# Kernel tuning notes

Hardware: AMD Instinct MI355X
Metric: run time of the kernel (lower is better)

## Reference

```python
import jax, jax.numpy as jnp
import numpy as np

N, C, E, B, NPG, MAX_LEN, H, EF = 16384, 512, 524288, 64, 256, 512, 8, 16
EPS = 1e-5

def layernorm(x, g, b):
    m = jnp.mean(x, axis=-1, keepdims=True)
    v = jnp.mean(jnp.square(x - m), axis=-1, keepdims=True)
    return (x - m) / jnp.sqrt(v + EPS) * g + b

def setup_inputs() -> dict:
    key = jax.random.key(0)
    ks = list(jax.random.split(key, 32))
    x = jax.random.normal(ks[0], (N, C), dtype=jnp.float32)
    edge_attr = jax.random.normal(ks[1], (E, EF), dtype=jnp.float32)
    # edges within each graph of NPG nodes
    src = jax.random.randint(ks[2], (E,), 0, N)
    dst = (src // NPG) * NPG + jax.random.randint(ks[3], (E,), 0, NPG)
    edge_index = jnp.stack([src, dst]).astype(jnp.int64)
    batch = jnp.repeat(jnp.arange(B), NPG).astype(jnp.int64)  # sorted graph ids
    s = 0.03
    p = lambda k, shp: jax.random.normal(k, shp, dtype=jnp.float32) * s
    return dict(
        x=x, edge_attr=edge_attr,
        gcn_w=p(ks[4], (C, C)), gcn_b=jnp.zeros((C,)),
        ep_w=p(ks[5], (EF, C)), ep_b=jnp.zeros((C,)),
        gate_w=p(ks[6], (2 * C, C)), gate_b=jnp.zeros((C,)),
        n1_g=jnp.ones((C,)), n1_b=jnp.zeros((C,)),
        in_w=p(ks[7], (C, 3 * C)), in_b=jnp.zeros((3 * C,)),
        out_w=p(ks[8], (C, C)), out_b=jnp.zeros((C,)),
        tn_g=jnp.ones((C,)), tn_b=jnp.zeros((C,)),
        m_w1=p(ks[9], (C, 2 * C)), m_b1=jnp.zeros((2 * C,)),
        m_w2=p(ks[10], (2 * C, C)), m_b2=jnp.zeros((C,)),
        fn_g=jnp.ones((C,)), fn_b=jnp.zeros((C,)),
        edge_index=edge_index, batch=batch,
    )

def reference(x, edge_attr, gcn_w, gcn_b, ep_w, ep_b, gate_w, gate_b,
              n1_g, n1_b, in_w, in_b, out_w, out_b, tn_g, tn_b,
              m_w1, m_b1, m_w2, m_b2, fn_g, fn_b, edge_index, batch):
    src, dst = edge_index[0], edge_index[1]
    # --- CoGNN: weighted GCN conv (self-loops, sym norm) ---
    ew = jax.lax.stop_gradient(jnp.sqrt(jnp.sum(edge_attr * edge_attr, axis=-1)))
    loop = jnp.arange(N)
    src2 = jnp.concatenate([src, loop]); dst2 = jnp.concatenate([dst, loop])
    ew2 = jnp.concatenate([ew, jnp.ones((N,), ew.dtype)])
    deg = jax.ops.segment_sum(ew2, dst2, num_segments=N)
    dinv = jnp.where(deg > 0, jax.lax.rsqrt(jnp.maximum(deg, 1e-12)), 0.0)
    norm = dinv[src2] * ew2 * dinv[dst2]
    xw = x @ gcn_w
    x_conv = jax.ops.segment_sum(norm[:, None] * xw[src2], dst2, num_segments=N) + gcn_b
    # edge_proj -> scatter_add at source nodes (dropout = identity in eval)
    ef = jax.nn.relu(edge_attr @ ep_w + ep_b)
    ef = jax.ops.segment_sum(ef, src, num_segments=N)
    gate = jax.nn.sigmoid(jnp.concatenate([x_conv, ef], axis=-1) @ gate_w + gate_b)
    x1 = gate * x_conv + (1.0 - gate) * ef
    x1 = jax.nn.relu(layernorm(x1, n1_g, n1_b))
    x = x1 + x  # identity residual (in_channels == hidden_channels)
    # --- to_dense_batch ---
    counts = jax.ops.segment_sum(jnp.ones((N,), jnp.int32), batch, num_segments=B)
    starts = jnp.cumsum(counts) - counts
    pos = jnp.arange(N) - starts[batch]
    xd = jnp.zeros((B, MAX_LEN, C), x.dtype).at[batch, pos].set(x)
    maskd = jnp.zeros((B, MAX_LEN), bool).at[batch, pos].set(True)
    # --- MHA (batch_first, key_padding_mask = ~mask) ---
    Dh = C // H
    qkv = xd @ in_w + in_b
    q, k, v = jnp.split(qkv, 3, axis=-1)
    q = q.reshape(B, MAX_LEN, H, Dh); k = k.reshape(B, MAX_LEN, H, Dh); v = v.reshape(B, MAX_LEN, H, Dh)
    scores = jnp.einsum('blhd,bmhd->bhlm', q, k) / jnp.sqrt(jnp.asarray(Dh, x.dtype))
    scores = jnp.where(maskd[:, None, None, :], scores, -1e9)
    attn = jax.nn.softmax(scores, axis=-1)
    o = jnp.einsum('bhlm,bmhd->blhd', attn, v).reshape(B, MAX_LEN, C)
    o = o @ out_w + out_b
    x_global = o[batch, pos]  # undo dense batching: x_global[mask]
    x = layernorm(x + x_global, tn_g, tn_b)
    # --- MLP ---
    x = x + (jax.nn.silu(x @ m_w1 + m_b1) @ m_w2 + m_b2)
    return layernorm(x, fn_g, fn_b)
```

## Files before the change

kernel.cpp:

```cpp
#include <hip/hip_runtime.h>

#define NN 16384
#define CC 512
#define EE 524288
#define BB 64
#define HH 8
#define EFD 16
#define GEMAXE 10240

typedef __bf16 bf16_t;
typedef __bf16 bf16x4 __attribute__((ext_vector_type(4)));
typedef __bf16 bf16x8 __attribute__((ext_vector_type(8)));
typedef float f32x4v __attribute__((ext_vector_type(4)));

__device__ __forceinline__ float2 ldb2(const bf16_t* p) {
  unsigned w = *(const unsigned*)p;
  return make_float2(__uint_as_float(w << 16), __uint_as_float(w & 0xFFFF0000u));
}


__global__ void init_kernel(int* ghist, int* nid_src, bf16_t* eacsr) {
  int i = threadIdx.x;
  if (i < 64) ghist[i] = 0;
  if (i < 32) nid_src[EE + i] = -1;
  ((int*)(eacsr + (size_t)EE * 16))[i] = 0;
}

__global__ __launch_bounds__(256) void edge_pass1(const float* __restrict__ ea,
                                                  const int* __restrict__ dst,
                                                  float* __restrict__ ew, int* ghist) {
  __shared__ int h[64];
  int tid = threadIdx.x;
  if (tid < 64) h[tid] = 0;
  __syncthreads();
  int e = blockIdx.x * 256 + tid;
  const float4* p = (const float4*)(ea + (size_t)e * EFD);
  float s = 0.f;
#pragma unroll
  for (int i = 0; i < 4; ++i) {
    float4 v = p[i];
    s += v.x * v.x + v.y * v.y + v.z * v.z + v.w * v.w;
  }
  ew[e] = sqrtf(s);
  atomicAdd(&h[dst[e] >> 8], 1);
  __syncthreads();
  if (tid < 64 && h[tid]) atomicAdd(&ghist[tid], h[tid]);
}

__global__ void gexscan_kernel(const int* __restrict__ ghist, int* __restrict__ gstart,
                               int* __restrict__ gcur) {
  if (threadIdx.x == 0) {
    int s = 0;
    for (int g = 0; g < 64; ++g) { gstart[g] = s; gcur[g] = s; s += ghist[g]; }
    gstart[64] = s;
  }
}

__global__ __launch_bounds__(256) void graph_scatter_kernel(
    const int* __restrict__ src, const int* __restrict__ dst,
    const float* __restrict__ ew, int* gcur, int2* __restrict__ grec,
    float* __restrict__ ewg) {
  __shared__ int h[64], base[64], h2[64];
  int tid = threadIdx.x;
  if (tid < 64) { h[tid] = 0; h2[tid] = 0; }
  __syncthreads();
  int e0 = blockIdx.x * 2048;
  int gloc[8];
#pragma unroll
  for (int k = 0; k < 8; ++k) {
    gloc[k] = dst[e0 + k * 256 + tid] >> 8;
    atomicAdd(&h[gloc[k]], 1);
  }
  __syncthreads();
  if (tid < 64) base[tid] = h[tid] ? atomicAdd(&gcur[tid], h[tid]) : 0;
  __syncthreads();
#pragma unroll
  for (int k = 0; k < 8; ++k) {
    int e = e0 + k * 256 + tid;
    int g = gloc[k];
    int p = atomicAdd(&h2[g], 1);
    int pos = base[g] + p;
    int ls = src[e] & 255;
    int ld = dst[e] & 255;
    grec[pos] = make_int2(e | (ls << 19), ld);
    ewg[pos] = ew[e];
  }
}

__global__ __launch_bounds__(1024) void graph_sort2_kernel(
    const int2* __restrict__ grec, const float* __restrict__ ewg,
    const int* __restrict__ gstart, int* __restrict__ elist_src,
    int* __restrict__ nid_src, int* __restrict__ start_src,
    float2* __restrict__ dstrec, int* __restrict__ start_dst,
    float* __restrict__ dinv) {
  __shared__ int lbuf[GEMAXE];
  __shared__ unsigned short sl[GEMAXE];
  __shared__ float ewl[GEMAXE];
  __shared__ int h[256], hx[256], h2[256];
  __shared__ float fdinv[256];
  const int g = blockIdx.x & 63;
  const int tid = threadIdx.x;
  const int gs = gstart[g];
  const int cnt = gstart[g + 1] - gs;
  if (tid < 256) { h[tid] = 0; h2[tid] = 0; }
  __syncthreads();
  if (blockIdx.x < 64) {
    for (int i = tid; i < cnt; i += 1024) {
      int2 r = grec[gs + i];
      int ld = r.y;
      sl[i] = (unsigned short)(((r.x >> 19) & 255) | (ld << 8));
      ewl[i] = ewg[gs + i];
      atomicAdd(&h[ld], 1);
    }
    __syncthreads();
    int myc = (tid < 256) ? h[tid] : 0;
    for (int off = 1; off < 256; off <<= 1) {
      int v = (tid < 256 && tid >= off) ? h[tid - off] : 0;
      __syncthreads();
      if (tid < 256) h[tid] += v;
      __syncthreads();
    }
    if (tid < 256) {
      hx[tid] = h[tid] - myc;
      start_dst[g * 256 + tid] = gs + hx[tid];
    }
    if (g == 63 && tid == 0) start_dst[NN] = EE;
    __syncthreads();
    for (int i = tid; i < cnt; i += 1024) {
      int ld = sl[i] >> 8;
      int p = hx[ld] + atomicAdd(&h2[ld], 1);
      lbuf[p] = i;
    }
    __syncthreads();
    if (tid < 256) {
      float dg = 1.0f;
      int s0 = hx[tid], e0 = s0 + myc;
      for (int i = s0; i < e0; ++i) dg += ewl[lbuf[i]];
      float dv = rsqrtf(fmaxf(dg, 1e-12f));
      fdinv[tid] = dv;
      dinv[g * 256 + tid] = dv;
    }
    __syncthreads();
    for (int p = tid; p < cnt; p += 1024) {
      int i = lbuf[p];
      int ls = sl[i] & 255;
      dstrec[gs + p] = make_float2(fdinv[ls] * ewl[i], __int_as_float(g * 256 + ls));
    }
  } else {
    int* wb = (int*)ewl;
    for (int i = tid; i < cnt; i += 1024) {
      int w = grec[gs + i].x;
      wb[i] = w;
      atomicAdd(&h[w >> 19], 1);
    }
    __syncthreads();
    int myc = (tid < 256) ? h[tid] : 0;
    for (int off = 1; off < 256; off <<= 1) {
      int v = (tid < 256 && tid >= off) ? h[tid - off] : 0;
      __syncthreads();
      if (tid < 256) h[tid] += v;
      __syncthreads();
    }
    if (tid < 256) {
      hx[tid] = h[tid] - myc;
      start_src[g * 256 + tid] = gs + hx[tid];
    }
    if (g == 63 && tid == 0) start_src[NN] = EE;
    __syncthreads();
    for (int i = tid; i < cnt; i += 1024) {
      int w = wb[i];
      int ls = w >> 19;
      int p = hx[ls] + atomicAdd(&h2[ls], 1);
      lbuf[p] = w;
    }
    __syncthreads();
    for (int p = tid; p < cnt; p += 1024) {
      int w = lbuf[p];
      elist_src[gs + p] = w & 0x7FFFF;
      nid_src[gs + p] = g * 256 + (w >> 19);
    }
  }
}

__global__ void ea_gather_kernel(const float* __restrict__ ea,
                                 const int* __restrict__ elist,
                                 bf16_t* __restrict__ eacsr) {
  int idx = blockIdx.x * 256 + threadIdx.x;
  if (idx >= EE * 2) return;
  int pos = idx >> 1, half = idx & 1;
  int e = elist[pos];
  const f32x4v* p = (const f32x4v*)(ea + (size_t)e * EFD + half * 8);
  f32x4v u0 = p[0], u1 = p[1];
  bf16x8 f;
#pragma unroll
  for (int r = 0; r < 4; ++r) {
    f[r] = (bf16_t)u0[r];
    f[4 + r] = (bf16_t)u1[r];
  }
  *(bf16x8*)(eacsr + (size_t)pos * 16 + half * 8) = f;
}


__global__ void cvt_bf16_kernel(const float* __restrict__ in, bf16_t* __restrict__ out,
                                int n4) {
  int i = blockIdx.x * 256 + threadIdx.x;
  if (i >= n4) return;
  float4 v = ((const float4*)in)[i];
  bf16x4 o;
  o[0] = (bf16_t)v.x; o[1] = (bf16_t)v.y; o[2] = (bf16_t)v.z; o[3] = (bf16_t)v.w;
  ((bf16x4*)out)[i] = o;
}

__global__ __launch_bounds__(256) void wt_kernel(const float* __restrict__ W,
                                                 bf16_t* __restrict__ Wt, int K, int N) {
  __shared__ float tile[32][33];
  int bx = blockIdx.x * 32;
  int by = blockIdx.y * 32;
  int tx = threadIdx.x & 31, ty = threadIdx.x >> 5;
#pragma unroll
  for (int i = 0; i < 32; i += 8)
    tile[ty + i][tx] = W[(size_t)(by + ty + i) * N + bx + tx];
  __syncthreads();
#pragma unroll
  for (int i = 0; i < 32; i += 8)
    Wt[(size_t)(bx + ty + i) * K + by + tx] = (bf16_t)tile[tx][ty + i];
}

__global__ __launch_bounds__(256) void xconv_kernel(
    const bf16_t* __restrict__ xwb, const float* __restrict__ dinv,
    const float2* __restrict__ dstrec, const int* __restrict__ start,
    const float* __restrict__ gcn_b, bf16_t* __restrict__ xcb) {
  int i = blockIdx.x;
  int tid = threadIdx.x;
  int st = start[i], en = start[i + 1];
  float di = dinv[i];
  int c0 = tid * 2;
  __shared__ float2 scS[256];
  float2 xv = ldb2(xwb + (size_t)i * CC + c0);
  float sc = di * di;
  float a0 = sc * xv.x + gcn_b[c0];
  float a1 = sc * xv.y + gcn_b[c0 + 1];
  for (int p0 = st; p0 < en; p0 += 256) {
    int m = min(256, en - p0);
    __syncthreads();
    if (tid < m) {
      float2 r = dstrec[p0 + tid];
      scS[tid] = make_float2(r.x * di, r.y);
    }
    __syncthreads();
    for (int j = 0; j < m; ++j) {
      float2 scv = scS[j];
      int sn = __float_as_int(scv.y);
      float2 v = ldb2(xwb + (size_t)sn * CC + c0);
      a0 += scv.x * v.x;
      a1 += scv.x * v.y;
    }
  }
  xcb[(size_t)i * (2 * CC) + c0] = (bf16_t)a0;
  xcb[(size_t)i * (2 * CC) + c0 + 1] = (bf16_t)a1;
}

__global__ __launch_bounds__(256) void ef_mfma_kernel(
    const bf16_t* __restrict__ eacsr, const float* __restrict__ ep_w,
    const float* __restrict__ ep_b, const int* __restrict__ nid,
    const int* __restrict__ start, bf16_t* __restrict__ efb) {
  const int tid = threadIdx.x;
  const int lane = tid & 63;
  const int wv = tid >> 6;
  const int l15 = lane & 15;
  const int g = lane >> 4;
  const int n0 = blockIdx.x * 16;
  const int cbase = wv * 128;

  bf16x8 wfr[8];
#pragma unroll
  for (int t = 0; t < 8; ++t) {
    bf16x8 f = {};
    int c = cbase + t * 16 + l15;
    if (g < 2) {
#pragma unroll
      for (int j = 0; j < 8; ++j) f[j] = (bf16_t)ep_w[(g * 8 + j) * CC + c];
    } else if (g == 2) {
      f[0] = (bf16_t)ep_b[c];
    }
    wfr[t] = f;
  }

  const int st = start[n0];
  const int en = start[n0 + 16];
  const int tgt = n0 + l15;

  f32x4v eacc[8] = {};

  for (int cb = st; cb < en; cb += 32) {
    bf16x8 af[2];
#pragma unroll
    for (int mE = 0; mE < 2; ++mE) {
      bf16x8 f = {};
      if (g < 2) {
        f = *(const bf16x8*)(eacsr + (size_t)(cb + mE * 16 + l15) * 16 + g * 8);
      } else if (g == 2) {
        f[0] = (bf16_t)1.0f;
      }
      af[mE] = f;
    }
    int4 idlo = *(const int4*)(nid + cb + g * 4);
    int4 idhi = *(const int4*)(nid + cb + 16 + g * 4);
    bf16x8 sf;
    sf[0] = (idlo.x == tgt) ? (bf16_t)1.0f : (bf16_t)0.0f;
    sf[1] = (idlo.y == tgt) ? (bf16_t)1.0f : (bf16_t)0.0f;
    sf[2] = (idlo.z == tgt) ? (bf16_t)1.0f : (bf16_t)0.0f;
    sf[3] = (idlo.w == tgt) ? (bf16_t)1.0f : (bf16_t)0.0f;
    sf[4] = (idhi.x == tgt) ? (bf16_t)1.0f : (bf16_t)0.0f;
    sf[5] = (idhi.y == tgt) ? (bf16_t)1.0f : (bf16_t)0.0f;
    sf[6] = (idhi.z == tgt) ? (bf16_t)1.0f : (bf16_t)0.0f;
    sf[7] = (idhi.w == tgt) ? (bf16_t)1.0f : (bf16_t)0.0f;
#pragma unroll
    for (int t = 0; t < 8; ++t) {
      f32x4v s0 = {}, s1 = {};
      s0 = __builtin_amdgcn_mfma_f32_16x16x32_bf16(af[0], wfr[t], s0, 0, 0, 0);
      s1 = __builtin_amdgcn_mfma_f32_16x16x32_bf16(af[1], wfr[t], s1, 0, 0, 0);
      union { bf16x8 v; bf16x4 h[2]; } pf;
#pragma unroll
      for (int r = 0; r < 4; ++r) {
        pf.h[0][r] = (bf16_t)fmaxf(s0[r], 0.f);
        pf.h[1][r] = (bf16_t)fmaxf(s1[r], 0.f);
      }
      eacc[t] = __builtin_amdgcn_mfma_f32_16x16x32_bf16(sf, pf.v, eacc[t], 0, 0, 0);
    }
  }
#pragma unroll
  for (int t = 0; t < 8; ++t) {
    int c = cbase + t * 16 + l15;
#pragma unroll
    for (int r = 0; r < 4; ++r) {
      int node = n0 + g * 4 + r;
      efb[(size_t)node * (2 * CC) + CC + c] = (bf16_t)eacc[t][r];
    }
  }
}

__device__ __forceinline__ void gl_lds16(const bf16_t* g, bf16_t* l) {
  __builtin_amdgcn_global_load_lds(
      (const __attribute__((address_space(1))) void*)g,
      (__attribute__((address_space(3))) void*)l, 16, 0, 0);
}

template <int ACT, int OUT>
__global__ __launch_bounds__(256) void gemm_bf16_kernel(
    const bf16_t* __restrict__ A, const bf16_t* __restrict__ Bt,
    const float* __restrict__ bias, void* __restrict__ Cout, int M, int N, int K) {
  __shared__ __align__(16) bf16_t Al[128 * 32];
  __shared__ __align__(16) bf16_t Bl[128 * 32];
  const int tid = threadIdx.x;
  const int lane = tid & 63;
  const int wave = tid >> 6;
  const int row0 = blockIdx.y * 128;
  const int col0 = blockIdx.x * 128;
  const int wm = (wave >> 1) * 64;
  const int wn = (wave & 1) * 64;
  f32x4v acc[4][4] = {};
  const bf16_t* aBase = A + (size_t)(row0 + (tid >> 2)) * K + (tid & 3) * 8;
  const bf16_t* bBase = Bt + (size_t)(col0 + (tid >> 2)) * K + (tid & 3) * 8;
  bf16_t* al0 = Al + wave * 512;
  bf16_t* al1 = Al + 2048 + wave * 512;
  bf16_t* bl0 = Bl + wave * 512;
  bf16_t* bl1 = Bl + 2048 + wave * 512;
  const int fr = lane & 15;
  const int fk = (lane >> 4) * 8;
  for (int k0 = 0; k0 < K; k0 += 32) {
    gl_lds16(aBase + k0, al0);
    gl_lds16(aBase + (size_t)64 * K + k0, al1);
    gl_lds16(bBase + k0, bl0);
    gl_lds16(bBase + (size_t)64 * K + k0, bl1);
    __syncthreads();
    bf16x8 af[4], bfv[4];
#pragma unroll
    for (int m = 0; m < 4; ++m)
      af[m] = *(const bf16x8*)(Al + (wm + m * 16 + fr) * 32 + fk);
#pragma unroll
    for (int n = 0; n < 4; ++n)
      bfv[n] = *(const bf16x8*)(Bl + (wn + n * 16 + fr) * 32 + fk);
#pragma unroll
    for (int m = 0; m < 4; ++m)
#pragma unroll
      for (int n = 0; n < 4; ++n)
        acc[m][n] =
            __builtin_amdgcn_mfma_f32_16x16x32_bf16(af[m], bfv[n], acc[m][n], 0, 0, 0);
    __syncthreads();
  }
  const int fq = (lane >> 4) * 4;
#pragma unroll
  for (int m = 0; m < 4; ++m) {
    int grb = row0 + wm + m * 16 + fq;
#pragma unroll
    for (int n = 0; n < 4; ++n) {
      int gc = col0 + wn + n * 16 + fr;
      float bv = bias ? bias[gc] : 0.f;
#pragma unroll
      for (int r = 0; r < 4; ++r) {
        float v = acc[m][n][r] + bv;
        if (ACT == 1) v = v / (1.f + __expf(-v));
        if (OUT == 0)
          ((float*)Cout)[(size_t)(grb + r) * N + gc] = v;
        else
          ((bf16_t*)Cout)[(size_t)(grb + r) * N + gc] = (bf16_t)v;
      }
    }
  }
}


__device__ inline void block_reduce2(float& s, float& q, float* red) {
#pragma unroll
  for (int off = 32; off >= 1; off >>= 1) {
    s += __shfl_xor(s, off, 64);
    q += __shfl_xor(q, off, 64);
  }
  int wid = threadIdx.x >> 6;
  if ((threadIdx.x & 63) == 0) { red[wid * 2] = s; red[wid * 2 + 1] = q; }
  __syncthreads();
  s = red[0] + red[2] + red[4] + red[6];
  q = red[1] + red[3] + red[5] + red[7];
}

template <int IA, int IB, int WF>
__global__ __launch_bounds__(256) void ln_addT_kernel(
    const void* __restrict__ A, const void* __restrict__ Bv,
    const float* __restrict__ g, const float* __restrict__ be,
    float* __restrict__ outf, bf16_t* __restrict__ outb) {
  int row = blockIdx.x, tid = threadIdx.x, c0 = tid * 2;
  __shared__ float red[8];
  float2 a = IA ? ldb2((const bf16_t*)A + (size_t)row * CC + c0)
                : *(const float2*)((const float*)A + (size_t)row * CC + c0);
  float2 b = IB ? ldb2((const bf16_t*)Bv + (size_t)row * CC + c0)
                : *(const float2*)((const float*)Bv + (size_t)row * CC + c0);
  float x0 = a.x + b.x, x1 = a.y + b.y;
  float s = x0 + x1, q = x0 * x0 + x1 * x1;
  block_reduce2(s, q, red);
  float mean = s * (1.f / CC);
  float var = q * (1.f / CC) - mean * mean;
  float rs = rsqrtf(var + 1e-5f);
  float o0 = (x0 - mean) * rs * g[c0] + be[c0];
  float o1 = (x1 - mean) * rs * g[c0 + 1] + be[c0 + 1];
  if (WF) {
    *(float2*)(outf + (size_t)row * CC + c0) = make_float2(o0, o1);
  } else {
    outb[(size_t)row * CC + c0] = (bf16_t)o0;
    outb[(size_t)row * CC + c0 + 1] = (bf16_t)o1;
  }
}

__global__ __launch_bounds__(256) void ln_gate_kernel(
    const bf16_t* __restrict__ gpreb, const float* __restrict__ gate_b,
    const bf16_t* __restrict__ xcef, const float* __restrict__ n1g,
    const float* __restrict__ n1b, const float* __restrict__ xin,
    bf16_t* __restrict__ x2b) {
  int row = blockIdx.x, tid = threadIdx.x, c0 = tid * 2;
  __shared__ float red[8];
  float2 gp = ldb2(gpreb + (size_t)row * CC + c0);
  float2 xcv = ldb2(xcef + (size_t)row * (2 * CC) + c0);
  float2 efv = ldb2(xcef + (size_t)row * (2 * CC) + CC + c0);
  float g0 = 1.f / (1.f + __expf(-(gp.x + gate_b[c0])));
  float g1 = 1.f / (1.f + __expf(-(gp.y + gate_b[c0 + 1])));
  float x0 = g0 * xcv.x + (1.f - g0) * efv.x;
  float x1 = g1 * xcv.y + (1.f - g1) * efv.y;
  float s = x0 + x1, q = x0 * x0 + x1 * x1;
  block_reduce2(s, q, red);
  float mean = s * (1.f / CC);
  float var = q * (1.f / CC) - mean * mean;
  float rs = rsqrtf(var + 1e-5f);
  float2 xi = *(const float2*)(xin + (size_t)row * CC + c0);
  float o0 = fmaxf((x0 - mean) * rs * n1g[c0] + n1b[c0], 0.f) + xi.x;
  float o1 = fmaxf((x1 - mean) * rs * n1g[c0 + 1] + n1b[c0 + 1], 0.f) + xi.y;
  x2b[(size_t)row * CC + c0] = (bf16_t)o0;
  x2b[(size_t)row * CC + c0 + 1] = (bf16_t)o1;
}

__global__ __launch_bounds__(256) void vt_pack_kernel(const bf16_t* __restrict__ qkvb,
                                                      bf16_t* __restrict__ vt) {
  int b = blockIdx.x >> 3, h = blockIdx.x & 7;
  int nb = b * 256;
  size_t voff = 1024 + (size_t)h * 64;
  char* out = (char*)(vt + (size_t)blockIdx.x * (64 * 256));
  __shared__ bf16_t tile[64][80];
  int tid = threadIdx.x;
  for (int kb = 0; kb < 4; ++kb) {
    __syncthreads();
#pragma unroll
    for (int p = 0; p < 2; ++p) {
      int k = p * 32 + (tid >> 3);
      int d8 = tid & 7;
      bf16x8 v = *(const bf16x8*)(qkvb + (size_t)(nb + kb * 64 + k) * 1536 + voff + d8 * 8);
      *(bf16x8*)(&tile[k][d8 * 8]) = v;
    }
    __syncthreads();
#pragma unroll
    for (int p = 0; p < 2; ++p) {
      int d = p * 32 + (tid >> 3);
      int k8 = tid & 7;
      bf16x8 v;
#pragma unroll
      for (int j = 0; j < 8; ++j) {
        int pos = k8 * 8 + j;
        int sl = pos & 31;
        int srck = (pos & 32) + ((sl >> 3) << 2) + (sl & 3) + (((sl >> 2) & 1) << 4);
        v[j] = tile[srck][d];
      }
      int byteoff = d * 512 + ((kb * 128 + k8 * 16) ^ ((d & 7) << 4));
      *(bf16x8*)(out + byteoff) = v;
    }
  }
}

__global__ __launch_bounds__(256, 2) void attn_mfma_kernel(
    const bf16_t* __restrict__ qkvb, const bf16_t* __restrict__ vt,
    bf16_t* __restrict__ o) {
  const int b = blockIdx.x >> 3;
  const int h = blockIdx.x & 7;
  const int nb = b * 256;
  const int tid = threadIdx.x;
  const int lane = tid & 63;
  const int wv = tid >> 6;
  const int l15 = lane & 15;
  const int g = lane >> 4;
  const int swzk = (l15 & 7) << 4;
  __shared__ __align__(16) bf16_t Klds[256 * 64];
  __shared__ __align__(16) bf16_t Vtlds[64 * 256];
  const size_t qoff = (size_t)h * 64;
  const size_t koff = 512 + (size_t)h * 64;

  {
    const int dcol = 16 * ((tid & 7) ^ ((tid >> 3) & 7));
    const bf16_t* srcb = qkvb + koff + (dcol >> 1);
#pragma unroll
    for (int i = 0; i < 8; ++i) {
      int k = i * 32 + (tid >> 3);
      gl_lds16(srcb + (size_t)(nb + k) * 1536, Klds + ((i * 4096 + wv * 1024) >> 1));
    }
  }
  {
    const bf16_t* vsrc = vt + (size_t)blockIdx.x * (64 * 256);
#pragma unroll
    for (int i = 0; i < 8; ++i) {
      int base = i * 4096 + wv * 1024;
      gl_lds16(vsrc + ((base >> 1) + lane * 8), Vtlds + (base >> 1));
    }
  }

  bf16x8 qf[4][2];
#pragma unroll
  for (int n = 0; n < 4; ++n) {
    const bf16_t* qp = qkvb + (size_t)(nb + wv * 64 + 16 * n + l15) * 1536 + qoff + g * 8;
    qf[n][0] = *(const bf16x8*)(qp);
    qf[n][1] = *(const bf16x8*)(qp + 32);
  }

  __syncthreads();

  f32x4v oacc[4][4] = {};
  float mrun[4] = {-1e30f, -1e30f, -1e30f, -1e30f};
  float lrun[4] = {0.f, 0.f, 0.f, 0.f};

  for (int kc = 0; kc < 4; ++kc) {
    f32x4v sacc[4][4] = {};
    const int kb128 = (kc * 64 + l15) * 128;
#pragma unroll
    for (int m = 0; m < 4; ++m) {
      bf16x8 a0 = *(const bf16x8*)(Klds + ((kb128 + m * 2048 + ((g * 16) ^ swzk)) >> 1));
      bf16x8 a1 =
          *(const bf16x8*)(Klds + ((kb128 + m * 2048 + ((64 + g * 16) ^ swzk)) >> 1));
#pragma unroll
      for (int n = 0; n < 4; ++n) {
        sacc[m][n] = __builtin_amdgcn_mfma_f32_16x16x32_bf16(a0, qf[n][0], sacc[m][n], 0, 0, 0);
        sacc[m][n] = __builtin_amdgcn_mfma_f32_16x16x32_bf16(a1, qf[n][1], sacc[m][n], 0, 0, 0);
      }
    }
    uint2 pb[4][4];
#pragma unroll
    for (int n = 0; n < 4; ++n) {
      float mx = sacc[0][n][0];
#pragma unroll
      for (int m = 0; m < 4; ++m)
#pragma unroll
        for (int r = 0; r < 4; ++r) mx = fmaxf(mx, sacc[m][n][r]);
      mx = fmaxf(mx, __shfl_xor(mx, 16));
      mx = fmaxf(mx, __shfl_xor(mx, 32));
      float mnew = fmaxf(mrun[n], mx);
      float c = __expf((mrun[n] - mnew) * 0.125f);
      mrun[n] = mnew;
      float s = 0.f;
#pragma unroll
      for (int m = 0; m < 4; ++m) {
        float p0 = __expf((sacc[m][n][0] - mnew) * 0.125f);
        float p1 = __expf((sacc[m][n][1] - mnew) * 0.125f);
        float p2 = __expf((sacc[m][n][2] - mnew) * 0.125f);
        float p3 = __expf((sacc[m][n][3] - mnew) * 0.125f);
        s += (p0 + p1) + (p2 + p3);
        union { bf16x4 v; uint2 u; } cv;
        cv.v[0] = (bf16_t)p0; cv.v[1] = (bf16_t)p1;
        cv.v[2] = (bf16_t)p2; cv.v[3] = (bf16_t)p3;
        pb[m][n] = cv.u;
      }
      s += __shfl_xor(s, 16);
      s += __shfl_xor(s, 32);
      lrun[n] = lrun[n] * c + s;
#pragma unroll
      for (int m = 0; m < 4; ++m)
#pragma unroll
        for (int r = 0; r < 4; ++r) oacc[m][n][r] *= c;
    }
#pragma unroll
    for (int h2 = 0; h2 < 2; ++h2) {
      bf16x8 vf[4];
#pragma unroll
      for (int m = 0; m < 4; ++m)
        vf[m] = *(const bf16x8*)(Vtlds + (((16 * m + l15) * 512 +
                                          ((kc * 128 + h2 * 64 + g * 16) ^ swzk)) >> 1));
#pragma unroll
      for (int n = 0; n < 4; ++n) {
        union { uint2 u[2]; bf16x8 v; } pf;
        pf.u[0] = pb[2 * h2][n];
        pf.u[1] = pb[2 * h2 + 1][n];
#pragma unroll
        for (int m = 0; m < 4; ++m)
          oacc[m][n] =
              __builtin_amdgcn_mfma_f32_16x16x32_bf16(vf[m], pf.v, oacc[m][n], 0, 0, 0);
      }
    }
  }
  float inv[4];
#pragma unroll
  for (int n = 0; n < 4; ++n) inv[n] = 1.0f / lrun[n];
#pragma unroll
  for (int m = 0; m < 4; ++m)
#pragma unroll
    for (int n = 0; n < 4; ++n) {
      bf16x4 pk;
#pragma unroll
      for (int r = 0; r < 4; ++r) pk[r] = (bf16_t)(oacc[m][n][r] * inv[n]);
      *(bf16x4*)(o + (size_t)(nb + wv * 64 + 16 * n + l15) * 512 + h * 64 + 16 * m +
                 4 * g) = pk;
    }
}


static inline char* alignp(char* p, size_t a) {
  return (char*)(((uintptr_t)p + a - 1) & ~(uintptr_t)(a - 1));
}

extern "C" void kernel_launch(void* const* d_in, const int* in_sizes, int n_in,
                              void* d_out, int out_size, void* d_ws, size_t ws_size,
                              hipStream_t stream) {
  const float* x = (const float*)d_in[0];
  const float* edge_attr = (const float*)d_in[1];
  const float* gcn_w = (const float*)d_in[2];
  const float* gcn_b = (const float*)d_in[3];
  const float* ep_w = (const float*)d_in[4];
  const float* ep_b = (const float*)d_in[5];
  const float* gate_w = (const float*)d_in[6];
  const float* gate_b = (const float*)d_in[7];
  const float* n1_g = (const float*)d_in[8];
  const float* n1_b = (const float*)d_in[9];
  const float* in_w = (const float*)d_in[10];
  const float* in_b = (const float*)d_in[11];
  const float* out_w = (const float*)d_in[12];
  const float* out_b = (const float*)d_in[13];
  const float* tn_g = (const float*)d_in[14];
  const float* tn_b = (const float*)d_in[15];
  const float* m_w1 = (const float*)d_in[16];
  const float* m_b1 = (const float*)d_in[17];
  const float* m_w2 = (const float*)d_in[18];
  const float* m_b2 = (const float*)d_in[19];
  const float* fn_g = (const float*)d_in[20];
  const float* fn_b = (const float*)d_in[21];
  const int* eidx = (const int*)d_in[22];
  const int* src = eidx;
  const int* dst = eidx + EE;

  float* ws = (float*)d_ws;
  float* R1 = ws;
  float* R2 = R1 + (size_t)NN * 3 * CC;
  float* R3 = R2 + (size_t)NN * CC;
  float* R4 = R3 + (size_t)NN * CC;
  float* ew = R4 + (size_t)NN * CC;
  float* dinv = ew + EE;
  int* ip = (int*)(dinv + NN);
  int* ghist = ip;      ip += 64;
  int* gstart = ip;     ip += 65;
  int* gcur = ip;       ip += 64;
  int* elist_src = ip;  ip += EE;
  int* nid_src = ip;    ip += EE + 32;
  int* start_src = ip;  ip += NN + 1;
  int* start_dst = ip;  ip += NN + 1;
  char* bp = alignp((char*)ip, 64);
  int2* grec = (int2*)bp;             bp += (size_t)EE * 8;
  float* ewg = (float*)bp;            bp += (size_t)EE * 4;
  float2* dstrec = (float2*)bp;       bp += (size_t)EE * 8;
  bf16_t* x2b = (bf16_t*)bp;          bp += (size_t)NN * CC * 2;
  bf16_t* gcn_wt = (bf16_t*)bp;       bp += (size_t)CC * CC * 2;
  bf16_t* gate_wt = (bf16_t*)bp;      bp += (size_t)CC * 2 * CC * 2;
  bf16_t* in_wt = (bf16_t*)bp;        bp += (size_t)3 * CC * CC * 2;
  bf16_t* out_wt = (bf16_t*)bp;       bp += (size_t)CC * CC * 2;
  bf16_t* m_w1t = (bf16_t*)bp;        bp += (size_t)2 * CC * CC * 2;
  bf16_t* m_w2t = (bf16_t*)bp;        bp += (size_t)CC * 2 * CC * 2;

  bf16_t* xb = (bf16_t*)R1;
  bf16_t* xcefb = (bf16_t*)R1;
  bf16_t* qkvb = (bf16_t*)R1;
  bf16_t* hb = (bf16_t*)R1;
  bf16_t* eacsr = (bf16_t*)((char*)R1 + (size_t)64 * 1024 * 1024);
  bf16_t* xwb = (bf16_t*)R2;
  bf16_t* gpreb = (bf16_t*)R2;
  bf16_t* ob = (bf16_t*)R2;
  bf16_t* vt = ob + (size_t)NN * CC;
  bf16_t* x3b = (bf16_t*)R2;
  bf16_t* oprjb = (bf16_t*)R4;
  float* yf = R4;

  init_kernel<<<1, 256, 0, stream>>>(ghist, nid_src, eacsr);
  edge_pass1<<<EE / 256, 256, 0, stream>>>(edge_attr, dst, ew, ghist);
  gexscan_kernel<<<1, 64, 0, stream>>>(ghist, gstart, gcur);
  graph_scatter_kernel<<<EE / 2048, 256, 0, stream>>>(src, dst, ew, gcur, grec, ewg);
  graph_sort2_kernel<<<128, 1024, 0, stream>>>(grec, ewg, gstart, elist_src, nid_src,
                                               start_src, dstrec, start_dst, dinv);
  ea_gather_kernel<<<(EE * 2 + 255) / 256, 256, 0, stream>>>(edge_attr, elist_src,
                                                             eacsr);

  wt_kernel<<<dim3(CC / 32, CC / 32), 256, 0, stream>>>(gcn_w, gcn_wt, CC, CC);
  wt_kernel<<<dim3(CC / 32, 2 * CC / 32), 256, 0, stream>>>(gate_w, gate_wt, 2 * CC, CC);
  wt_kernel<<<dim3(3 * CC / 32, CC / 32), 256, 0, stream>>>(in_w, in_wt, CC, 3 * CC);
  wt_kernel<<<dim3(CC / 32, CC / 32), 256, 0, stream>>>(out_w, out_wt, CC, CC);
  wt_kernel<<<dim3(2 * CC / 32, CC / 32), 256, 0, stream>>>(m_w1, m_w1t, CC, 2 * CC);
  wt_kernel<<<dim3(CC / 32, 2 * CC / 32), 256, 0, stream>>>(m_w2, m_w2t, 2 * CC, CC);

  cvt_bf16_kernel<<<(NN * CC / 4 + 255) / 256, 256, 0, stream>>>(x, xb, NN * CC / 4);
  dim3 gA(CC / 128, NN / 128);
  gemm_bf16_kernel<0, 1><<<gA, 256, 0, stream>>>(xb, gcn_wt, nullptr, xwb, NN, CC, CC);
  xconv_kernel<<<NN, 256, 0, stream>>>(xwb, dinv, dstrec, start_dst, gcn_b, xcefb);
  ef_mfma_kernel<<<NN / 16, 256, 0, stream>>>(eacsr, ep_w, ep_b, nid_src, start_src,
                                              xcefb);
  gemm_bf16_kernel<0, 1><<<gA, 256, 0, stream>>>(xcefb, gate_wt, nullptr, gpreb, NN,
                                                 CC, 2 * CC);
  ln_gate_kernel<<<NN, 256, 0, stream>>>(gpreb, gate_b, xcefb, n1_g, n1_b, x, x2b);

  dim3 gQ(3 * CC / 128, NN / 128);
  gemm_bf16_kernel<0, 1><<<gQ, 256, 0, stream>>>(x2b, in_wt, in_b, qkvb, NN, 3 * CC, CC);
  vt_pack_kernel<<<BB * HH, 256, 0, stream>>>(qkvb, vt);
  attn_mfma_kernel<<<BB * HH, 256, 0, stream>>>(qkvb, vt, ob);
  gemm_bf16_kernel<0, 1><<<gA, 256, 0, stream>>>(ob, out_wt, out_b, oprjb, NN, CC, CC);
  ln_addT_kernel<1, 1, 0><<<NN, 256, 0, stream>>>(x2b, oprjb, tn_g, tn_b, nullptr, x3b);

  dim3 gH(2 * CC / 128, NN / 128);
  gemm_bf16_kernel<1, 1><<<gH, 256, 0, stream>>>(x3b, m_w1t, m_b1, hb, NN, 2 * CC, CC);
  gemm_bf16_kernel<0, 0><<<gA, 256, 0, stream>>>(hb, m_w2t, m_b2, yf, NN, CC, 2 * CC);
  ln_addT_kernel<1, 0, 1><<<NN, 256, 0, stream>>>(x3b, yf, fn_g, fn_b, (float*)d_out,
                                                  nullptr);
}
```

Baseline: 485.9 us.

## Replace sparse GCN gather with dense per-graph normalized adjacency GEMM

Builds a dense 256x256 normalized adjacency block per graph (including self-loop weights) in LDS, writes it as bf16, and computes the GCN aggregation as a block-diagonal MFMA GEMM against a transposed xw. This replaces the per-node gather kernel with its irregular row loads. The precomputed edge record now stores the full symmetric norm and a local source index. The edge-feature kernel is also retiled to 512 threads with 64 columns per wave. The cost is extra dense work, bf16 rounding of adjacency weights, and a transposed xw GEMM.

```diff
diff --git a/kernel.cpp b/kernel.cpp
--- a/kernel.cpp
+++ b/kernel.cpp
@@ -144,7 +144,9 @@
     for (int p = tid; p < cnt; p += 1024) {
       int i = lbuf[p];
       int ls = sl[i] & 255;
-      dstrec[gs + p] = make_float2(fdinv[ls] * ewl[i], __int_as_float(g * 256 + ls));
+      int ld = sl[i] >> 8;
+      dstrec[gs + p] =
+          make_float2(fdinv[ls] * ewl[i] * fdinv[ld], __int_as_float(ls));
     }
   } else {
     int* wb = (int*)ewl;
@@ -200,6 +202,39 @@
   *(bf16x8*)(eacsr + (size_t)pos * 16 + half * 8) = f;
 }
 
+__global__ __launch_bounds__(256) void an_build_kernel(
+    const float2* __restrict__ dstrec, const int* __restrict__ start_dst,
+    const float* __restrict__ dinv, bf16_t* __restrict__ An) {
+  __shared__ float AnS[128][256];
+  const int g = blockIdx.x >> 1, h = blockIdx.x & 1;
+  const int tid = threadIdx.x;
+  float4* az = (float4*)&AnS[0][0];
+  for (int i = tid; i < 128 * 256 / 4; i += 256)
+    az[i] = make_float4(0.f, 0.f, 0.f, 0.f);
+  __syncthreads();
+  const int nbase = g * 256 + h * 128;
+  if (tid < 128) {
+    int node = nbase + tid;
+    int st = start_dst[node], en = start_dst[node + 1];
+    float* row = AnS[tid];
+    for (int p = st; p < en; ++p) {
+      float2 r = dstrec[p];
+      row[__float_as_int(r.y)] += r.x;
+    }
+    float dv = dinv[node];
+    row[h * 128 + tid] += dv * dv;
+  }
+  __syncthreads();
+  bf16_t* out = An + (size_t)nbase * 256;
+  const float* s0 = &AnS[0][0];
+  for (int i = tid; i < 128 * 256 / 8; i += 256) {
+    bf16x8 v;
+#pragma unroll
+    for (int r = 0; r < 8; ++r) v[r] = (bf16_t)s0[i * 8 + r];
+    *(bf16x8*)(out + i * 8) = v;
+  }
+}
+
 
 __global__ void cvt_bf16_kernel(const float* __restrict__ in, bf16_t* __restrict__ out,
                                 int n4) {
@@ -226,41 +261,7 @@
     Wt[(size_t)(bx + ty + i) * K + by + tx] = (bf16_t)tile[tx][ty + i];
 }
 
-__global__ __launch_bounds__(256) void xconv_kernel(
-    const bf16_t* __restrict__ xwb, const float* __restrict__ dinv,
-    const float2* __restrict__ dstrec, const int* __restrict__ start,
-    const float* __restrict__ gcn_b, bf16_t* __restrict__ xcb) {
-  int i = blockIdx.x;
-  int tid = threadIdx.x;
-  int st = start[i], en = start[i + 1];
-  float di = dinv[i];
-  int c0 = tid * 2;
-  __shared__ float2 scS[256];
-  float2 xv = ldb2(xwb + (size_t)i * CC + c0);
-  float sc = di * di;
-  float a0 = sc * xv.x + gcn_b[c0];
-  float a1 = sc * xv.y + gcn_b[c0 + 1];
-  for (int p0 = st; p0 < en; p0 += 256) {
-    int m = min(256, en - p0);
-    __syncthreads();
-    if (tid < m) {
-      float2 r = dstrec[p0 + tid];
-      scS[tid] = make_float2(r.x * di, r.y);
-    }
-    __syncthreads();
-    for (int j = 0; j < m; ++j) {
-      float2 scv = scS[j];
-      int sn = __float_as_int(scv.y);
-      float2 v = ldb2(xwb + (size_t)sn * CC + c0);
-      a0 += scv.x * v.x;
-      a1 += scv.x * v.y;
-    }
-  }
-  xcb[(size_t)i * (2 * CC) + c0] = (bf16_t)a0;
-  xcb[(size_t)i * (2 * CC) + c0 + 1] = (bf16_t)a1;
-}
-
-__global__ __launch_bounds__(256) void ef_mfma_kernel(
+__global__ __launch_bounds__(512) void ef_mfma_kernel(
     const bf16_t* __restrict__ eacsr, const float* __restrict__ ep_w,
     const float* __restrict__ ep_b, const int* __restrict__ nid,
     const int* __restrict__ start, bf16_t* __restrict__ efb) {
@@ -270,11 +271,11 @@
   const int l15 = lane & 15;
   const int g = lane >> 4;
   const int n0 = blockIdx.x * 16;
-  const int cbase = wv * 128;
-
-  bf16x8 wfr[8];
-#pragma unroll
-  for (int t = 0; t < 8; ++t) {
+  const int cbase = wv * 64;
+
+  bf16x8 wfr[4];
+#pragma unroll
+  for (int t = 0; t < 4; ++t) {
     bf16x8 f = {};
     int c = cbase + t * 16 + l15;
     if (g < 2) {
@@ -290,7 +291,7 @@
   const int en = start[n0 + 16];
   const int tgt = n0 + l15;
 
-  f32x4v eacc[8] = {};
+  f32x4v eacc[4] = {};
 
   for (int cb = st; cb < en; cb += 32) {
     bf16x8 af[2];
@@ -316,7 +317,7 @@
     sf[6] = (idhi.z == tgt) ? (bf16_t)1.0f : (bf16_t)0.0f;
     sf[7] = (idhi.w == tgt) ? (bf16_t)1.0f : (bf16_t)0.0f;
 #pragma unroll
-    for (int t = 0; t < 8; ++t) {
+    for (int t = 0; t < 4; ++t) {
       f32x4v s0 = {}, s1 = {};
       s0 = __builtin_amdgcn_mfma_f32_16x16x32_bf16(af[0], wfr[t], s0, 0, 0, 0);
       s1 = __builtin_amdgcn_mfma_f32_16x16x32_bf16(af[1], wfr[t], s1, 0, 0, 0);
@@ -330,7 +331,7 @@
     }
   }
 #pragma unroll
-  for (int t = 0; t < 8; ++t) {
+  for (int t = 0; t < 4; ++t) {
     int c = cbase + t * 16 + l15;
 #pragma unroll
     for (int r = 0; r < 4; ++r) {
@@ -406,6 +407,65 @@
         else
           ((bf16_t*)Cout)[(size_t)(grb + r) * N + gc] = (bf16_t)v;
       }
+    }
+  }
+}
+
+__global__ __launch_bounds__(256) void an_gemm_kernel(
+    const bf16_t* __restrict__ An, const bf16_t* __restrict__ xwT,
+    const float* __restrict__ bias, bf16_t* __restrict__ outb) {
+  __shared__ __align__(16) bf16_t Al[128 * 32];
+  __shared__ __align__(16) bf16_t Bl[128 * 32];
+  const int tid = threadIdx.x;
+  const int lane = tid & 63;
+  const int wave = tid >> 6;
+  const int row0 = blockIdx.y * 128;
+  const int col0 = blockIdx.x * 128;
+  const int g = row0 >> 8;
+  f32x4v acc[4][4] = {};
+  const bf16_t* aBase = An + (size_t)(row0 + (tid >> 2)) * 256 + (tid & 3) * 8;
+  const bf16_t* bBase =
+      xwT + (size_t)(col0 + (tid >> 2)) * NN + g * 256 + (tid & 3) * 8;
+  bf16_t* al0 = Al + wave * 512;
+  bf16_t* al1 = Al + 2048 + wave * 512;
+  bf16_t* bl0 = Bl + wave * 512;
+  bf16_t* bl1 = Bl + 2048 + wave * 512;
+  const int wm = (wave >> 1) * 64;
+  const int wn = (wave & 1) * 64;
+  const int fr = lane & 15;
+  const int fk = (lane >> 4) * 8;
+  for (int k0 = 0; k0 < 256; k0 += 32) {
+    gl_lds16(aBase + k0, al0);
+    gl_lds16(aBase + (size_t)64 * 256 + k0, al1);
+    gl_lds16(bBase + k0, bl0);
+    gl_lds16(bBase + (size_t)64 * NN + k0, bl1);
+    __syncthreads();
+    bf16x8 af[4], bfv[4];
+#pragma unroll
+    for (int m = 0; m < 4; ++m)
+      af[m] = *(const bf16x8*)(Al + (wm + m * 16 + fr) * 32 + fk);
+#pragma unroll
+    for (int n = 0; n < 4; ++n)
+      bfv[n] = *(const bf16x8*)(Bl + (wn + n * 16 + fr) * 32 + fk);
+#pragma unroll
+    for (int m = 0; m < 4; ++m)
+#pragma unroll
+      for (int n = 0; n < 4; ++n)
+        acc[m][n] =
+            __builtin_amdgcn_mfma_f32_16x16x32_bf16(af[m], bfv[n], acc[m][n], 0, 0, 0);
+    __syncthreads();
+  }
+  const int fq = (lane >> 4) * 4;
+#pragma unroll
+  for (int m = 0; m < 4; ++m) {
+    int grb = row0 + wm + m * 16 + fq;
+#pragma unroll
+    for (int n = 0; n < 4; ++n) {
+      int gc = col0 + wn + n * 16 + fr;
+      float bv = bias[gc];
+#pragma unroll
+      for (int r = 0; r < 4; ++r)
+        outb[(size_t)(grb + r) * (2 * CC) + gc] = (bf16_t)(acc[m][n][r] + bv);
     }
   }
 }
@@ -710,11 +770,12 @@
   bf16_t* qkvb = (bf16_t*)R1;
   bf16_t* hb = (bf16_t*)R1;
   bf16_t* eacsr = (bf16_t*)((char*)R1 + (size_t)64 * 1024 * 1024);
-  bf16_t* xwb = (bf16_t*)R2;
+  bf16_t* xwT = (bf16_t*)R2;
   bf16_t* gpreb = (bf16_t*)R2;
   bf16_t* ob = (bf16_t*)R2;
   bf16_t* vt = ob + (size_t)NN * CC;
   bf16_t* x3b = (bf16_t*)R2;
+  bf16_t* AnFull = (bf16_t*)R3;
   bf16_t* oprjb = (bf16_t*)R4;
   float* yf = R4;
 
@@ -726,6 +787,7 @@
                                                start_src, dstrec, start_dst, dinv);
   ea_gather_kernel<<<(EE * 2 + 255) / 256, 256, 0, stream>>>(edge_attr, elist_src,
                                                              eacsr);
+  an_build_kernel<<<128, 256, 0, stream>>>(dstrec, start_dst, dinv, AnFull);
 
   wt_kernel<<<dim3(CC / 32, CC / 32), 256, 0, stream>>>(gcn_w, gcn_wt, CC, CC);
   wt_kernel<<<dim3(CC / 32, 2 * CC / 32), 256, 0, stream>>>(gate_w, gate_wt, 2 * CC, CC);
@@ -735,11 +797,13 @@
   wt_kernel<<<dim3(CC / 32, 2 * CC / 32), 256, 0, stream>>>(m_w2, m_w2t, 2 * CC, CC);
 
   cvt_bf16_kernel<<<(NN * CC / 4 + 255) / 256, 256, 0, stream>>>(x, xb, NN * CC / 4);
+  gemm_bf16_kernel<0, 1><<<dim3(NN / 128, CC / 128), 256, 0, stream>>>(
+      gcn_wt, xb, nullptr, xwT, CC, NN, CC);
+  an_gemm_kernel<<<dim3(CC / 128, NN / 128), 256, 0, stream>>>(AnFull, xwT, gcn_b,
+                                                               xcefb);
+  ef_mfma_kernel<<<NN / 16, 512, 0, stream>>>(eacsr, ep_w, ep_b, nid_src, start_src,
+                                              xcefb);
   dim3 gA(CC / 128, NN / 128);
-  gemm_bf16_kernel<0, 1><<<gA, 256, 0, stream>>>(xb, gcn_wt, nullptr, xwb, NN, CC, CC);
-  xconv_kernel<<<NN, 256, 0, stream>>>(xwb, dinv, dstrec, start_dst, gcn_b, xcefb);
-  ef_mfma_kernel<<<NN / 16, 256, 0, stream>>>(eacsr, ep_w, ep_b, nid_src, start_src,
-                                              xcefb);
   gemm_bf16_kernel<0, 1><<<gA, 256, 0, stream>>>(xcefb, gate_wt, nullptr, gpreb, NN,
                                                  CC, 2 * CC);
   ln_gate_kernel<<<NN, 256, 0, stream>>>(gpreb, gate_b, xcefb, n1_g, n1_b, x, x2b);
```

Result: faster. 472.9 us (-2.7%).
